# Kernel optimization log

Hardware: AMD Instinct MI355X
Metric: run time of the kernel (lower is better)

Reference implementation:

```python
import jax, jax.numpy as jnp
import numpy as np

D = 256; H = 8; DK = D // H
NT, NW, ND = 2000, 50000, 20000
E_TT, E_WT, E_TD, E_WD = 128000, 256000, 320000, 320000
SQRT_DK = float(np.sqrt(DK))


def setup_inputs() -> dict:
    key = jax.random.key(0)
    ks = jax.random.split(key, 32)
    def nrm(i, shape, s=0.05):
        return jax.random.normal(ks[i], shape, jnp.float32) * s
    inp = {
        "feat_topic": nrm(0, (NT, D), 1.0),
        "feat_word": nrm(1, (NW, D), 1.0),
        "feat_doc": nrm(2, (ND, D), 1.0),
        "ht_prev": nrm(3, (NT, D), 1.0),
        # stacked per-ntype linears, index: 0=topic, 1=word, 2=doc
        "Wk": nrm(4, (3, D, D)), "bk": nrm(5, (3, D)),
        "Wq": nrm(6, (3, D, D)), "bq": nrm(7, (3, D)),
        "Wv": nrm(8, (3, D, D)), "bv": nrm(9, (3, D)),
        # a_linears, index: 0=topic, 1=doc
        "Wa": nrm(10, (2, D, D)), "ba": nrm(11, (2, D)),
        "ln_g": jnp.ones((2, D), jnp.float32),
        "ln_b": jnp.zeros((2, D), jnp.float32),
        "skip": jnp.ones((2,), jnp.float32),
        # RNNCell for topic
        "Wih": nrm(12, (D, D)), "Whh": nrm(13, (D, D)),
        "bih": nrm(14, (D,)), "bhh": nrm(15, (D,)),
        # relation params, index: 0=tt, 1=wt, 2=td, 3=wd
        "rel_pri": jnp.ones((4, H), jnp.float32),
        "rel_att": nrm(16, (4, H, DK, DK), 0.1),
        "rel_msg": nrm(17, (4, H, DK, DK), 0.1),
        "src_tt": jax.random.randint(ks[18], (E_TT,), 0, NT),
        "dst_tt": jnp.arange(E_TT, dtype=jnp.int32) % NT,
        "src_wt": jax.random.randint(ks[19], (E_WT,), 0, NW),
        "dst_wt": jnp.arange(E_WT, dtype=jnp.int32) % NT,
        "src_td": jax.random.randint(ks[20], (E_TD,), 0, NT),
        "dst_td": jnp.arange(E_TD, dtype=jnp.int32) % ND,
        "src_wd": jax.random.randint(ks[21], (E_WD,), 0, NW),
        "dst_wd": jnp.arange(E_WD, dtype=jnp.int32) % ND,
    }
    return inp


def _proj(x, W, b):
    return (x @ W + b).reshape(-1, H, DK)


def _layernorm(x, g, b):
    mu = x.mean(-1, keepdims=True)
    var = ((x - mu) ** 2).mean(-1, keepdims=True)
    return (x - mu) * jax.lax.rsqrt(var + 1e-5) * g + b


def _rel_message(k, v, q, src, dst, pri, A_att, A_msg, n_dst):
    # k,v: [N_src,H,DK]; q: [N_dst,H,DK]; per-edge gather-compute-scatter
    key = jnp.einsum('ehd,hdo->eho', k[src], A_att)          # [E,H,DK]
    att = (q[dst] * key).sum(-1) * pri / SQRT_DK             # [E,H]
    val = jnp.einsum('ehd,hdo->eho', v[src], A_msg)          # [E,H,DK]
    m = jax.ops.segment_max(att, dst, num_segments=n_dst)
    e = jnp.exp(att - m[dst])
    s = jax.ops.segment_sum(e, dst, num_segments=n_dst)
    a = e / s[dst]                                           # edge softmax per dst
    t = jax.ops.segment_sum(a[..., None] * val, dst, num_segments=n_dst)
    return jax.nn.relu(t.reshape(n_dst, D))


def reference(feat_topic, feat_word, feat_doc, ht_prev, Wk, bk, Wq, bq, Wv, bv,
              Wa, ba, ln_g, ln_b, skip, Wih, Whh, bih, bhh,
              rel_pri, rel_att, rel_msg,
              src_tt, dst_tt, src_wt, dst_wt, src_td, dst_td, src_wd, dst_wd):
    # ---- phase 1: messages into topic nodes (etypes tt, wt) ----
    k_t = _proj(feat_topic, Wk[0], bk[0]); v_t = _proj(feat_topic, Wv[0], bv[0])
    k_w = _proj(feat_word,  Wk[1], bk[1]); v_w = _proj(feat_word,  Wv[1], bv[1])
    q_t = _proj(feat_topic, Wq[0], bq[0])
    t_tt = _rel_message(k_t, v_t, q_t, src_tt, dst_tt, rel_pri[0], rel_att[0], rel_msg[0], NT)
    t_wt = _rel_message(k_w, v_w, q_t, src_wt, dst_wt, rel_pri[1], rel_att[1], rel_msg[1], NT)
    t_topic = 0.5 * (t_tt + t_wt)                            # cross_reducer='mean'
    alpha = jax.nn.sigmoid(skip[0])
    trans = t_topic @ Wa[0] + ba[0]
    mix = trans * alpha + feat_topic * (1.0 - alpha)
    h = jnp.tanh(mix @ Wih + bih + ht_prev @ Whh + bhh)      # RNNCell
    topic_out = _layernorm(h, ln_g[0], ln_b[0])
    # ---- phase 2: messages into doc nodes (etypes td, wd), topic uses updated feats ----
    k_t2 = _proj(topic_out, Wk[0], bk[0]); v_t2 = _proj(topic_out, Wv[0], bv[0])
    q_d = _proj(feat_doc, Wq[2], bq[2])
    t_td = _rel_message(k_t2, v_t2, q_d, src_td, dst_td, rel_pri[2], rel_att[2], rel_msg[2], ND)
    t_wd = _rel_message(k_w, v_w, q_d, src_wd, dst_wd, rel_pri[3], rel_att[3], rel_msg[3], ND)
    t_doc = 0.5 * (t_td + t_wd)
    alpha2 = jax.nn.sigmoid(skip[1])
    trans2 = t_doc @ Wa[1] + ba[1]
    mix2 = trans2 * alpha2 + feat_doc * (1.0 - alpha2)
    doc_out = _layernorm(mix2, ln_g[1], ln_b[1])
    return topic_out, doc_out
```

## Files before the change

kernel.cpp:

```cpp
#include <hip/hip_runtime.h>
#include <hip/hip_bf16.h>
#include <hip/hip_fp8.h>

typedef __attribute__((ext_vector_type(8))) short bf16x8;
typedef __attribute__((ext_vector_type(4))) float f32x4;
typedef __attribute__((ext_vector_type(2))) float f32x2;

constexpr int NT = 2000, NW = 50000, ND = 20000;
constexpr float INV_SQRT_DK = 0.17677669529663687f;

__device__ inline float bfu(unsigned short u) {
    return __uint_as_float(((unsigned int)u) << 16);
}
__device__ inline float blo(unsigned int u) { return __uint_as_float(u << 16); }
__device__ inline float bhi(unsigned int u) { return __uint_as_float(u & 0xffff0000u); }
__device__ inline short f2bf(float x) {
    __hip_bfloat16 h = __float2bfloat16(x);
    short s; __builtin_memcpy(&s, &h, 2); return s;
}

__device__ inline void dec4(unsigned int w, float* o) {
#if __has_builtin(__builtin_amdgcn_cvt_pk_f32_fp8)
    f32x2 a = __builtin_amdgcn_cvt_pk_f32_fp8(w, false);
    f32x2 b = __builtin_amdgcn_cvt_pk_f32_fp8(w, true);
    o[0] = a[0]; o[1] = a[1]; o[2] = b[0]; o[3] = b[1];
#else
    __hip_fp8_e4m3 t0, t1, t2, t3;
    t0.__x = (__hip_fp8_storage_t)(w & 0xff);
    t1.__x = (__hip_fp8_storage_t)((w >> 8) & 0xff);
    t2.__x = (__hip_fp8_storage_t)((w >> 16) & 0xff);
    t3.__x = (__hip_fp8_storage_t)((w >> 24) & 0xff);
    o[0] = (float)t0; o[1] = (float)t1; o[2] = (float)t2; o[3] = (float)t3;
#endif
}
__device__ inline unsigned char f2fp8(float v) {
#if __has_builtin(__builtin_amdgcn_cvt_pk_fp8_f32)
    return (unsigned char)(__builtin_amdgcn_cvt_pk_fp8_f32(v, v, 0u, false) & 0xff);
#else
    __hip_fp8_e4m3 h(v); return (unsigned char)h.__x;
#endif
}

__device__ inline void cstore(float* p, float v) { *p = v; }
__device__ inline void cstore(short* p, float v) { *p = f2bf(v); }
__device__ inline void cstore(unsigned char* p, float v) { *p = f2fp8(v); }

__device__ inline void gload16(const short* g, short* l) {
    __builtin_amdgcn_global_load_lds(
        (const __attribute__((address_space(1))) void*)g,
        (__attribute__((address_space(3))) void*)l, 16, 0, 0);
}

__device__ inline float dot32f8(const unsigned char* __restrict__ kp, const float* __restrict__ qh) {
    const uint4 u = *reinterpret_cast<const uint4*>(kp);
    const uint4 v = *reinterpret_cast<const uint4*>(kp + 16);
    const unsigned int ws[8] = {u.x, u.y, u.z, u.w, v.x, v.y, v.z, v.w};
    float d = 0.f;
    #pragma unroll
    for (int c = 0; c < 8; ++c) {
        float f[4];
        dec4(ws[c], f);
        d += qh[c * 4 + 0] * f[0] + qh[c * 4 + 1] * f[1]
           + qh[c * 4 + 2] * f[2] + qh[c * 4 + 3] * f[3];
    }
    return d;
}

__global__ __launch_bounds__(256) void fold_kernel(
    const float* __restrict__ Wk, const float* __restrict__ bk,
    const float* __restrict__ Wv, const float* __restrict__ bv,
    const float* __restrict__ rel_att, const float* __restrict__ rel_msg,
    short* __restrict__ B_t1, short* __restrict__ B_w, short* __restrict__ B_t2,
    float* __restrict__ bias_t1, float* __restrict__ bias_w, float* __restrict__ bias_t2)
{
    const int f = blockIdx.x >> 3, chunk = blockIdx.x & 7;
    const int rel = f >> 1, isV = f & 1;
    const int ntype = (rel == 1 || rel == 3) ? 1 : 0;
    const float* Wsrc = (isV ? Wv : Wk) + ntype * 65536;
    const float* bsrc = (isV ? bv : bk) + ntype * 256;
    const float* A    = (isV ? rel_msg : rel_att) + rel * 8192;
    short* wdst; float* bdst;
    switch (f) {
        case 0: wdst = B_t1 + 65536;     bdst = bias_t1 + 256; break;
        case 1: wdst = B_t1 + 2 * 65536; bdst = bias_t1 + 512; break;
        case 2: wdst = B_w;              bdst = bias_w;        break;
        case 3: wdst = B_w + 65536;      bdst = bias_w + 256;  break;
        case 4: wdst = B_t2;             bdst = bias_t2;       break;
        case 5: wdst = B_t2 + 65536;     bdst = bias_t2 + 256; break;
        case 6: wdst = B_w + 2 * 65536;  bdst = bias_w + 512;  break;
        default: wdst = B_w + 3 * 65536; bdst = bias_w + 768;  break;
    }
    __shared__ float Wsh[32][256];
    const int tid = threadIdx.x;
    for (int i = 0; i < 32; ++i)
        Wsh[i][tid] = Wsrc[(chunk * 32 + i) * 256 + tid];
    __syncthreads();
    const int h = tid >> 5, o = tid & 31;
    float a[32];
    #pragma unroll
    for (int d = 0; d < 32; ++d) a[d] = A[h * 1024 + d * 32 + o];
    short tmp[32];
    #pragma unroll
    for (int r = 0; r < 32; ++r) {
        float s = 0.f;
        #pragma unroll
        for (int d = 0; d < 32; ++d) s = fmaf(Wsh[r][(h << 5) + d], a[d], s);
        tmp[r] = f2bf(s);
    }
    short* wp = wdst + tid * 256 + chunk * 32;
    #pragma unroll
    for (int r8 = 0; r8 < 4; ++r8) {
        bf16x8 v;
        #pragma unroll
        for (int t = 0; t < 8; ++t) v[t] = tmp[r8 * 8 + t];
        *reinterpret_cast<bf16x8*>(wp + r8 * 8) = v;
    }
    if (chunk == 0) {
        float s = 0.f;
        #pragma unroll
        for (int d = 0; d < 32; ++d) s = fmaf(bsrc[(h << 5) + d], a[d], s);
        bdst[tid] = s;
    }
}

struct TransP { const float* s[6]; short* d[6]; };
__global__ __launch_bounds__(256) void wtrans6(TransP p) {
    const int m = blockIdx.y, n = blockIdx.x, k = threadIdx.x;
    p.d[m][n * 256 + k] = f2bf(p.s[m][k * 256 + n]);
}

__global__ void copy_bias(const float* __restrict__ s, float* __restrict__ d) {
    d[threadIdx.x] = s[threadIdx.x];
}

template <bool XF32, typename OutT, int EPI, bool SWZ>
__global__ __launch_bounds__(256) void gemm_lds(
    const void* __restrict__ Xv, const short* __restrict__ Wt,
    const float* __restrict__ bias, OutT* __restrict__ C,
    int M, int ldc, const float* __restrict__ extra,
    const float* __restrict__ skipv, int skipIdx)
{
    __shared__ short As[128 * 64];
    __shared__ short Bs[128 * 64];
    int bxi = blockIdx.x, byi = blockIdx.y;
    if constexpr (SWZ) {
        const int h = bxi + (int)gridDim.x * byi;
        const int i = h >> 3;
        byi = (h & 7) + 8 * (i >> 3);
        bxi = i & 7;
        if (byi * 128 >= M) return;
    }
    const int tid = threadIdx.x;
    const int wave = tid >> 6, lane = tid & 63;
    const int wm = wave >> 1, wn = wave & 1;
    const int r = lane & 15, kb = lane >> 4;
    const int col0 = bxi * 128;
    const int row0 = byi * 128;

    const int l8 = lane >> 3;
    const int c8 = lane & 7;
    const int swz8 = c8 ^ l8;
    f32x4 acc[4][4] = {};

    for (int k0 = 0; k0 < 256; k0 += 64) {
        if (k0) __syncthreads();
        if constexpr (XF32) {
            #pragma unroll
            for (int q = 0; q < 4; ++q) {
                const int rl = wave * 32 + q * 8 + l8;
                const int grow = min(row0 + rl, M - 1);
                const float* xp = (const float*)Xv + grow * 256 + k0 + c8 * 8;
                const float4 x0 = *reinterpret_cast<const float4*>(xp);
                const float4 x1 = *reinterpret_cast<const float4*>(xp + 4);
                bf16x8 v;
                v[0] = f2bf(x0.x); v[1] = f2bf(x0.y); v[2] = f2bf(x0.z); v[3] = f2bf(x0.w);
                v[4] = f2bf(x1.x); v[5] = f2bf(x1.y); v[6] = f2bf(x1.z); v[7] = f2bf(x1.w);
                *reinterpret_cast<bf16x8*>(As + rl * 64 + swz8 * 8) = v;
            }
        } else {
            #pragma unroll
            for (int q = 0; q < 4; ++q) {
                const int rl = wave * 32 + q * 8 + l8;
                const int grow = min(row0 + rl, M - 1);
                gload16((const short*)Xv + grow * 256 + k0 + swz8 * 8,
                        As + (wave * 32 + q * 8) * 64);
            }
        }
        #pragma unroll
        for (int q = 0; q < 4; ++q) {
            const int cl = wave * 32 + q * 8 + l8;
            gload16(Wt + (col0 + cl) * 256 + k0 + swz8 * 8,
                    Bs + (wave * 32 + q * 8) * 64);
        }
        __syncthreads();
        #pragma unroll
        for (int s = 0; s < 2; ++s) {
            const int csw = ((kb + 4 * s) ^ (r & 7)) * 8;
            bf16x8 af[4], bw[4];
            #pragma unroll
            for (int i = 0; i < 4; ++i) {
                af[i] = *reinterpret_cast<const bf16x8*>(As + (wm * 64 + i * 16 + r) * 64 + csw);
                bw[i] = *reinterpret_cast<const bf16x8*>(Bs + (wn * 64 + i * 16 + r) * 64 + csw);
            }
            #pragma unroll
            for (int i = 0; i < 4; ++i)
                #pragma unroll
                for (int j = 0; j < 4; ++j)
                    acc[i][j] = __builtin_amdgcn_mfma_f32_16x16x32_bf16(af[i], bw[j], acc[i][j], 0, 0, 0);
        }
    }

    float alpha = 0.f;
    if (EPI == 1) alpha = 1.f / (1.f + __expf(-skipv[skipIdx]));
    #pragma unroll
    for (int i = 0; i < 4; ++i) {
        #pragma unroll
        for (int j = 0; j < 4; ++j) {
            const int col = col0 + wn * 64 + j * 16 + r;
            const float bc = bias[col];
            #pragma unroll
            for (int t = 0; t < 4; ++t) {
                const int rrow = row0 + wm * 64 + i * 16 + kb * 4 + t;
                if (rrow < M) {
                    float v = acc[i][j][t] + bc;
                    if (EPI == 1) v = alpha * v + (1.f - alpha) * extra[rrow * 256 + col];
                    if (EPI == 2) v = tanhf(v + extra[rrow * 256 + col]);
                    cstore(C + rrow * ldc + col, v);
                }
            }
        }
    }
}

template <int NE>
__device__ inline void rel_scores_f8(const unsigned char* __restrict__ kv, int ld, int koff,
                                     const int* __restrict__ sidx, int off, float scale,
                                     const float* __restrict__ qh, float* __restrict__ sc,
                                     int g, int l)
{
    constexpr int NL = NE / 32;
    float att[NL];
    #pragma unroll
    for (int t = 0; t < NL; ++t)
        att[t] = dot32f8(kv + (size_t)sidx[off + l + 32 * t] * ld + koff + g * 32, qh) * scale;
    float m = att[0];
    #pragma unroll
    for (int t = 1; t < NL; ++t) m = fmaxf(m, att[t]);
    #pragma unroll
    for (int o = 16; o > 0; o >>= 1) m = fmaxf(m, __shfl_xor(m, o));
    float ex[NL], s = 0.f;
    #pragma unroll
    for (int t = 0; t < NL; ++t) { ex[t] = __expf(att[t] - m); s += ex[t]; }
    #pragma unroll
    for (int o = 16; o > 0; o >>= 1) s += __shfl_xor(s, o);
    const float inv = 1.f / s;
    #pragma unroll
    for (int t = 0; t < NL; ++t) sc[(off + l + 32 * t) * 9 + g] = ex[t] * inv;
}

template <int NE>
__device__ inline void accum_f8(const unsigned char* __restrict__ kv, int ld, int voff,
                                const int* __restrict__ sidx, int off,
                                const float* __restrict__ sc,
                                int es, int ct, int h, float* __restrict__ acc)
{
    #pragma unroll
    for (int e = es; e < NE; e += 8) {
        const float w = sc[(off + e) * 9 + h];
        const uint2 u = *reinterpret_cast<const uint2*>(
            kv + (size_t)sidx[off + e] * ld + voff + ct * 8);
        float f[8];
        dec4(u.x, f); dec4(u.y, f + 4);
        #pragma unroll
        for (int k = 0; k < 8; ++k) acc[k] = fmaf(w, f[k], acc[k]);
    }
}

template <int NEA, int NEB>
__global__ __launch_bounds__(256) void msg_k(
    const short* __restrict__ q, int ldq,
    const unsigned char* __restrict__ kvA, int ldA, int koffA, int voffA,
    const int* __restrict__ srcA,
    const unsigned char* __restrict__ kvB, int ldB, int koffB, int voffB,
    const int* __restrict__ srcB,
    const float* __restrict__ relPri, int relA, int relB,
    short* __restrict__ out, int n_dst)
{
    constexpr int NET = NEA + NEB;
    const int j = blockIdx.x, tid = threadIdx.x;
    __shared__ float qsh[256];
    __shared__ int sidx[NET];
    __shared__ float sc[NET * 9];
    __shared__ float psA[8][256];
    __shared__ float psB[8][256];

    qsh[tid] = bfu((unsigned short)q[j * ldq + tid]);
    if (tid < NEA) sidx[tid] = srcA[j + tid * n_dst];
    else if (tid < NET) sidx[tid] = srcB[j + (tid - NEA) * n_dst];
    __syncthreads();

    const int g = tid >> 5, l = tid & 31;
    float qr[32];
    #pragma unroll
    for (int c = 0; c < 8; ++c) {
        const float4 v = *reinterpret_cast<const float4*>(qsh + g * 32 + c * 4);
        qr[c * 4] = v.x; qr[c * 4 + 1] = v.y; qr[c * 4 + 2] = v.z; qr[c * 4 + 3] = v.w;
    }

    if constexpr (NEA == 16 && NEB == 16) {
        const int isB = l >> 4;
        const unsigned char* base = isB ? kvB + koffB : kvA + koffA;
        const int ld = isB ? ldB : ldA;
        const float scale = relPri[(isB ? relB : relA) * 8 + g] * INV_SQRT_DK;
        const float att = dot32f8(base + (size_t)sidx[l] * ld + g * 32, qr) * scale;
        float m = att;
        #pragma unroll
        for (int o = 8; o > 0; o >>= 1) m = fmaxf(m, __shfl_xor(m, o));
        const float ex = __expf(att - m);
        float s = ex;
        #pragma unroll
        for (int o = 8; o > 0; o >>= 1) s += __shfl_xor(s, o);
        sc[l * 9 + g] = ex / s;
    } else {
        rel_scores_f8<NEA>(kvA, ldA, koffA, sidx, 0,
                           relPri[relA * 8 + g] * INV_SQRT_DK, qr, sc, g, l);
        rel_scores_f8<NEB>(kvB, ldB, koffB, sidx, NEA,
                           relPri[relB * 8 + g] * INV_SQRT_DK, qr, sc, g, l);
    }
    __syncthreads();

    const int es = tid >> 5, ct = tid & 31, hh = ct >> 2;
    float accA[8] = {}, accB[8] = {};
    accum_f8<NEA>(kvA, ldA, voffA, sidx, 0,   sc, es, ct, hh, accA);
    accum_f8<NEB>(kvB, ldB, voffB, sidx, NEA, sc, es, ct, hh, accB);
    const int sw = ct & 4;
    *reinterpret_cast<float4*>(&psA[es][(ct * 8) ^ sw])     = make_float4(accA[0], accA[1], accA[2], accA[3]);
    *reinterpret_cast<float4*>(&psA[es][(ct * 8 + 4) ^ sw]) = make_float4(accA[4], accA[5], accA[6], accA[7]);
    *reinterpret_cast<float4*>(&psB[es][(ct * 8) ^ sw])     = make_float4(accB[0], accB[1], accB[2], accB[3]);
    *reinterpret_cast<float4*>(&psB[es][(ct * 8 + 4) ^ sw]) = make_float4(accB[4], accB[5], accB[6], accB[7]);
    __syncthreads();

    float rA = 0.f, rB = 0.f;
    const int rp = tid ^ ((tid >> 3) & 4);
    #pragma unroll
    for (int e2 = 0; e2 < 8; ++e2) { rA += psA[e2][rp]; rB += psB[e2][rp]; }
    out[j * 256 + tid] = f2bf(0.5f * (fmaxf(rA, 0.f) + fmaxf(rB, 0.f)));
}

template <bool WB>
__global__ __launch_bounds__(256) void ln_k(
    float* __restrict__ data, const float* __restrict__ g,
    const float* __restrict__ b, int nrows, short* __restrict__ bfout)
{
    const int wid = threadIdx.x >> 6, lane = threadIdx.x & 63;
    const int row = blockIdx.x * 4 + wid;
    if (row >= nrows) return;
    float4 x = *reinterpret_cast<float4*>(data + row * 256 + lane * 4);
    float s  = x.x + x.y + x.z + x.w;
    float q2 = x.x * x.x + x.y * x.y + x.z * x.z + x.w * x.w;
    #pragma unroll
    for (int o = 32; o > 0; o >>= 1) { s += __shfl_xor(s, o); q2 += __shfl_xor(q2, o); }
    const float mu  = s * (1.f / 256.f);
    const float var = q2 * (1.f / 256.f) - mu * mu;
    const float rr = rsqrtf(var + 1e-5f);
    const float4 gg = *reinterpret_cast<const float4*>(g + lane * 4);
    const float4 bb = *reinterpret_cast<const float4*>(b + lane * 4);
    x.x = (x.x - mu) * rr * gg.x + bb.x;
    x.y = (x.y - mu) * rr * gg.y + bb.y;
    x.z = (x.z - mu) * rr * gg.z + bb.z;
    x.w = (x.w - mu) * rr * gg.w + bb.w;
    *reinterpret_cast<float4*>(data + row * 256 + lane * 4) = x;
    if (WB) {
        ushort4 u;
        u.x = (unsigned short)f2bf(x.x); u.y = (unsigned short)f2bf(x.y);
        u.z = (unsigned short)f2bf(x.z); u.w = (unsigned short)f2bf(x.w);
        *reinterpret_cast<ushort4*>((unsigned short*)bfout + row * 256 + lane * 4) = u;
    }
}

extern "C" void kernel_launch(void* const* d_in, const int* in_sizes, int n_in,
                              void* d_out, int out_size, void* d_ws, size_t ws_size,
                              hipStream_t stream)
{
    const float* feat_topic = (const float*)d_in[0];
    const float* feat_word  = (const float*)d_in[1];
    const float* feat_doc   = (const float*)d_in[2];
    const float* ht_prev    = (const float*)d_in[3];
    const float* Wk  = (const float*)d_in[4];
    const float* bk  = (const float*)d_in[5];
    const float* Wq  = (const float*)d_in[6];
    const float* bq  = (const float*)d_in[7];
    const float* Wv  = (const float*)d_in[8];
    const float* bv  = (const float*)d_in[9];
    const float* Wa  = (const float*)d_in[10];
    const float* ba  = (const float*)d_in[11];
    const float* ln_g = (const float*)d_in[12];
    const float* ln_b = (const float*)d_in[13];
    const float* skip = (const float*)d_in[14];
    const float* Wih  = (const float*)d_in[15];
    const float* Whh  = (const float*)d_in[16];
    const float* bih  = (const float*)d_in[17];
    const float* bhh  = (const float*)d_in[18];
    const float* rel_pri = (const float*)d_in[19];
    const float* rel_att = (const float*)d_in[20];
    const float* rel_msg = (const float*)d_in[21];
    const int* src_tt = (const int*)d_in[22];
    const int* src_wt = (const int*)d_in[24];
    const int* src_td = (const int*)d_in[26];
    const int* src_wd = (const int*)d_in[28];

    short* B_t1 = (short*)d_ws;
    short* B_w  = B_t1 + 196608;
    short* B_t2 = B_w + 262144;
    short* Wq2t = B_t2 + 131072;
    short* Whht = Wq2t + 65536;
    short* Wa0t = Whht + 65536;
    short* Wiht = Wa0t + 65536;
    short* Wa1t = Wiht + 65536;
    short* q_t  = Wa1t + 65536;
    unsigned char* kv1 = (unsigned char*)(q_t + 512000);
    unsigned char* w8  = kv1 + 1024000;
    unsigned char* kv2 = w8 + 51200000;
    short* qd   = (short*)(kv2 + 1024000);
    short* ttop = qd + 5120000;
    short* mixb = ttop + 512000;
    short* tdoc = mixb + 512000;
    short* xt2  = tdoc + 5120000;
    float* bias_t1 = (float*)(xt2 + 512000);
    float* bias_w  = bias_t1 + 768;
    float* bias_t2 = bias_w + 1024;
    float* r2      = bias_t2 + 512;

    float* out_topic = (float*)d_out;
    float* out_doc   = out_topic + NT * 256;

    fold_kernel<<<dim3(64), 256, 0, stream>>>(Wk, bk, Wv, bv, rel_att, rel_msg,
                                              B_t1, B_w, B_t2, bias_t1, bias_w, bias_t2);
    TransP tp;
    tp.s[0] = Wq;            tp.d[0] = B_t1;
    tp.s[1] = Wq + 131072;   tp.d[1] = Wq2t;
    tp.s[2] = Whh;           tp.d[2] = Whht;
    tp.s[3] = Wih;           tp.d[3] = Wiht;
    tp.s[4] = Wa;            tp.d[4] = Wa0t;
    tp.s[5] = Wa + 65536;    tp.d[5] = Wa1t;
    wtrans6<<<dim3(256, 6), 256, 0, stream>>>(tp);
    copy_bias<<<dim3(1), 256, 0, stream>>>(bq, bias_t1);

    gemm_lds<true, unsigned char, 0, true><<<dim3(8, 392), 256, 0, stream>>>(
        feat_word, B_w, bias_w, w8, NW, 1024, nullptr, nullptr, 0);

    gemm_lds<true, short, 0, false><<<dim3(2, 16), 256, 0, stream>>>(
        feat_topic, B_t1, bias_t1, q_t, NT, 256, nullptr, nullptr, 0);
    gemm_lds<true, unsigned char, 0, false><<<dim3(4, 16), 256, 0, stream>>>(
        feat_topic, B_t1 + 65536, bias_t1 + 256, kv1, NT, 512, nullptr, nullptr, 0);
    gemm_lds<true, short, 0, false><<<dim3(2, 157), 256, 0, stream>>>(
        feat_doc, Wq2t, bq + 512, qd, ND, 256, nullptr, nullptr, 0);
    gemm_lds<true, float, 0, false><<<dim3(2, 16), 256, 0, stream>>>(
        ht_prev, Whht, bhh, r2, NT, 256, nullptr, nullptr, 0);

    msg_k<64, 128><<<dim3(NT), 256, 0, stream>>>(
        q_t, 256,
        kv1, 512, 0, 256, src_tt,
        w8, 1024, 0, 256, src_wt,
        rel_pri, 0, 1, ttop, NT);

    gemm_lds<false, short, 1, false><<<dim3(2, 16), 256, 0, stream>>>(
        ttop, Wa0t, ba, mixb, NT, 256, feat_topic, skip, 0);
    gemm_lds<false, float, 2, false><<<dim3(2, 16), 256, 0, stream>>>(
        mixb, Wiht, bih, out_topic, NT, 256, r2, nullptr, 0);
    ln_k<true><<<dim3(500), 256, 0, stream>>>(out_topic, ln_g, ln_b, NT, xt2);

    gemm_lds<false, unsigned char, 0, false><<<dim3(4, 16), 256, 0, stream>>>(
        xt2, B_t2, bias_t2, kv2, NT, 512, nullptr, nullptr, 0);

    msg_k<16, 16><<<dim3(ND), 256, 0, stream>>>(
        qd, 256,
        kv2, 512, 0, 256, src_td,
        w8, 1024, 512, 768, src_wd,
        rel_pri, 2, 3, tdoc, ND);

    gemm_lds<false, float, 1, false><<<dim3(2, 157), 256, 0, stream>>>(
        tdoc, Wa1t, ba + 256, out_doc, ND, 256, feat_doc, skip, 1);
    ln_k<false><<<dim3(5000), 256, 0, stream>>>(out_doc, ln_g + 256, ln_b + 256, ND, nullptr);
}
```

Measured before the change: 311.6 us.

## Double-buffer LDS tiles in GEMM with register prefetch of next K-slice

Replaces the single-buffered 64-wide K-step GEMM with a double-buffered pipeline over 32-wide K-slices. Global loads for the next slice (async LDS loads for bf16, register prefetch for fp32 inputs) are issued before the MFMA work on the current buffer, with one barrier per step. The LDS layout changes to a smaller swizzle, and fp32 A tiles use padded rows. This aims to hide global memory latency behind compute, at the cost of more barriers per tile and more registers for the prefetch.

```diff
diff --git a/kernel.cpp b/kernel.cpp
--- a/kernel.cpp
+++ b/kernel.cpp
@@ -134,14 +134,15 @@
 }
 
 template <bool XF32, typename OutT, int EPI, bool SWZ>
-__global__ __launch_bounds__(256) void gemm_lds(
+__global__ __launch_bounds__(256) void gemm_db(
     const void* __restrict__ Xv, const short* __restrict__ Wt,
     const float* __restrict__ bias, OutT* __restrict__ C,
     int M, int ldc, const float* __restrict__ extra,
     const float* __restrict__ skipv, int skipIdx)
 {
-    __shared__ short As[128 * 64];
-    __shared__ short Bs[128 * 64];
+    constexpr int LDA = XF32 ? 36 : 32;
+    __shared__ short As[2][128 * LDA];
+    __shared__ short Bs[2][128 * 32];
     int bxi = blockIdx.x, byi = blockIdx.y;
     if constexpr (SWZ) {
         const int h = bxi + (int)gridDim.x * byi;
@@ -154,61 +155,91 @@
     const int wave = tid >> 6, lane = tid & 63;
     const int wm = wave >> 1, wn = wave & 1;
     const int r = lane & 15, kb = lane >> 4;
-    const int col0 = bxi * 128;
-    const int row0 = byi * 128;
-
-    const int l8 = lane >> 3;
-    const int c8 = lane & 7;
-    const int swz8 = c8 ^ l8;
+    const int col0 = bxi * 128, row0 = byi * 128;
+
+    const int srow = lane >> 2;
+    const int sc8  = lane & 3;
+    const int swz  = (lane >> 3) & 3;
+    const int gc8  = sc8 ^ swz;
+    const int rsw  = (r >> 1) & 3;
+    const int aslot = XF32 ? kb : (kb ^ rsw);
+    const int bslot = kb ^ rsw;
+
     f32x4 acc[4][4] = {};
-
-    for (int k0 = 0; k0 < 256; k0 += 64) {
-        if (k0) __syncthreads();
-        if constexpr (XF32) {
+    float4 pf[4];
+
+    auto stageB = [&](int t, int b) {
+        const int k0 = t * 32;
+        #pragma unroll
+        for (int q2 = 0; q2 < 2; ++q2) {
+            const int cl = wave * 32 + q2 * 16;
+            gload16(Wt + (col0 + cl + srow) * 256 + k0 + gc8 * 8,
+                    &Bs[b][cl * 32]);
+        }
+    };
+    auto stageA16 = [&](int t, int b) {
+        const int k0 = t * 32;
+        #pragma unroll
+        for (int q2 = 0; q2 < 2; ++q2) {
+            const int rl = wave * 32 + q2 * 16;
+            const int grow = min(row0 + rl + srow, M - 1);
+            gload16((const short*)Xv + grow * 256 + k0 + gc8 * 8,
+                    &As[b][rl * 32]);
+        }
+    };
+    auto stageAf_load = [&](int t) {
+        const int k0 = t * 32;
+        #pragma unroll
+        for (int q2 = 0; q2 < 2; ++q2) {
+            const int grow = min(row0 + wave * 32 + q2 * 16 + srow, M - 1);
+            const float* xp = (const float*)Xv + grow * 256 + k0 + sc8 * 8;
+            pf[q2 * 2]     = *reinterpret_cast<const float4*>(xp);
+            pf[q2 * 2 + 1] = *reinterpret_cast<const float4*>(xp + 4);
+        }
+    };
+    auto stageAf_write = [&](int b) {
+        #pragma unroll
+        for (int q2 = 0; q2 < 2; ++q2) {
+            const float4 x0 = pf[q2 * 2], x1 = pf[q2 * 2 + 1];
+            bf16x8 v;
+            v[0] = f2bf(x0.x); v[1] = f2bf(x0.y); v[2] = f2bf(x0.z); v[3] = f2bf(x0.w);
+            v[4] = f2bf(x1.x); v[5] = f2bf(x1.y); v[6] = f2bf(x1.z); v[7] = f2bf(x1.w);
+            *reinterpret_cast<bf16x8*>(
+                &As[b][(wave * 32 + q2 * 16 + srow) * 36 + sc8 * 8]) = v;
+        }
+    };
+    auto compute = [&](int b) {
+        bf16x8 af[4], bw[4];
+        #pragma unroll
+        for (int i = 0; i < 4; ++i) {
+            af[i] = *reinterpret_cast<const bf16x8*>(
+                &As[b][(wm * 64 + i * 16 + r) * LDA + aslot * 8]);
+            bw[i] = *reinterpret_cast<const bf16x8*>(
+                &Bs[b][(wn * 64 + i * 16 + r) * 32 + bslot * 8]);
+        }
+        #pragma unroll
+        for (int i = 0; i < 4; ++i)
             #pragma unroll
-            for (int q = 0; q < 4; ++q) {
-                const int rl = wave * 32 + q * 8 + l8;
-                const int grow = min(row0 + rl, M - 1);
-                const float* xp = (const float*)Xv + grow * 256 + k0 + c8 * 8;
-                const float4 x0 = *reinterpret_cast<const float4*>(xp);
-                const float4 x1 = *reinterpret_cast<const float4*>(xp + 4);
-                bf16x8 v;
-                v[0] = f2bf(x0.x); v[1] = f2bf(x0.y); v[2] = f2bf(x0.z); v[3] = f2bf(x0.w);
-                v[4] = f2bf(x1.x); v[5] = f2bf(x1.y); v[6] = f2bf(x1.z); v[7] = f2bf(x1.w);
-                *reinterpret_cast<bf16x8*>(As + rl * 64 + swz8 * 8) = v;
-            }
-        } else {
-            #pragma unroll
-            for (int q = 0; q < 4; ++q) {
-                const int rl = wave * 32 + q * 8 + l8;
-                const int grow = min(row0 + rl, M - 1);
-                gload16((const short*)Xv + grow * 256 + k0 + swz8 * 8,
-                        As + (wave * 32 + q * 8) * 64);
-            }
-        }
-        #pragma unroll
-        for (int q = 0; q < 4; ++q) {
-            const int cl = wave * 32 + q * 8 + l8;
-            gload16(Wt + (col0 + cl) * 256 + k0 + swz8 * 8,
-                    Bs + (wave * 32 + q * 8) * 64);
-        }
+            for (int j = 0; j < 4; ++j)
+                acc[i][j] = __builtin_amdgcn_mfma_f32_16x16x32_bf16(af[i], bw[j], acc[i][j], 0, 0, 0);
+    };
+
+    if constexpr (XF32) { stageAf_load(0); stageAf_write(0); }
+    else stageA16(0, 0);
+    stageB(0, 0);
+    __syncthreads();
+    int cur = 0;
+    #pragma unroll
+    for (int t = 0; t < 7; ++t) {
+        if constexpr (XF32) stageAf_load(t + 1);
+        stageB(t + 1, cur ^ 1);
+        if constexpr (!XF32) stageA16(t + 1, cur ^ 1);
+        compute(cur);
+        if constexpr (XF32) stageAf_write(cur ^ 1);
         __syncthreads();
-        #pragma unroll
-        for (int s = 0; s < 2; ++s) {
-            const int csw = ((kb + 4 * s) ^ (r & 7)) * 8;
-            bf16x8 af[4], bw[4];
-            #pragma unroll
-            for (int i = 0; i < 4; ++i) {
-                af[i] = *reinterpret_cast<const bf16x8*>(As + (wm * 64 + i * 16 + r) * 64 + csw);
-                bw[i] = *reinterpret_cast<const bf16x8*>(Bs + (wn * 64 + i * 16 + r) * 64 + csw);
-            }
-            #pragma unroll
-            for (int i = 0; i < 4; ++i)
-                #pragma unroll
-                for (int j = 0; j < 4; ++j)
-                    acc[i][j] = __builtin_amdgcn_mfma_f32_16x16x32_bf16(af[i], bw[j], acc[i][j], 0, 0, 0);
-        }
-    }
+        cur ^= 1;
+    }
+    compute(cur);
 
     float alpha = 0.f;
     if (EPI == 1) alpha = 1.f / (1.f + __expf(-skipv[skipIdx]));
@@ -446,16 +477,16 @@
     wtrans6<<<dim3(256, 6), 256, 0, stream>>>(tp);
     copy_bias<<<dim3(1), 256, 0, stream>>>(bq, bias_t1);
 
-    gemm_lds<true, unsigned char, 0, true><<<dim3(8, 392), 256, 0, stream>>>(
+    gemm_db<true, unsigned char, 0, true><<<dim3(8, 392), 256, 0, stream>>>(
         feat_word, B_w, bias_w, w8, NW, 1024, nullptr, nullptr, 0);
 
-    gemm_lds<true, short, 0, false><<<dim3(2, 16), 256, 0, stream>>>(
+    gemm_db<true, short, 0, false><<<dim3(2, 16), 256, 0, stream>>>(
         feat_topic, B_t1, bias_t1, q_t, NT, 256, nullptr, nullptr, 0);
-    gemm_lds<true, unsigned char, 0, false><<<dim3(4, 16), 256, 0, stream>>>(
+    gemm_db<true, unsigned char, 0, false><<<dim3(4, 16), 256, 0, stream>>>(
         feat_topic, B_t1 + 65536, bias_t1 + 256, kv1, NT, 512, nullptr, nullptr, 0);
-    gemm_lds<true, short, 0, false><<<dim3(2, 157), 256, 0, stream>>>(
+    gemm_db<true, short, 0, false><<<dim3(2, 157), 256, 0, stream>>>(
         feat_doc, Wq2t, bq + 512, qd, ND, 256, nullptr, nullptr, 0);
-    gemm_lds<true, float, 0, false><<<dim3(2, 16), 256, 0, stream>>>(
+    gemm_db<true, float, 0, false><<<dim3(2, 16), 256, 0, stream>>>(
         ht_prev, Whht, bhh, r2, NT, 256, nullptr, nullptr, 0);
 
     msg_k<64, 128><<<dim3(NT), 256, 0, stream>>>(
@@ -464,13 +495,13 @@
         w8, 1024, 0, 256, src_wt,
         rel_pri, 0, 1, ttop, NT);
 
-    gemm_lds<false, short, 1, false><<<dim3(2, 16), 256, 0, stream>>>(
+    gemm_db<false, short, 1, false><<<dim3(2, 16), 256, 0, stream>>>(
         ttop, Wa0t, ba, mixb, NT, 256, feat_topic, skip, 0);
-    gemm_lds<false, float, 2, false><<<dim3(2, 16), 256, 0, stream>>>(
+    gemm_db<false, float, 2, false><<<dim3(2, 16), 256, 0, stream>>>(
         mixb, Wiht, bih, out_topic, NT, 256, r2, nullptr, 0);
     ln_k<true><<<dim3(500), 256, 0, stream>>>(out_topic, ln_g, ln_b, NT, xt2);
 
-    gemm_lds<false, unsigned char, 0, false><<<dim3(4, 16), 256, 0, stream>>>(
+    gemm_db<false, unsigned char, 0, false><<<dim3(4, 16), 256, 0, stream>>>(
         xt2, B_t2, bias_t2, kv2, NT, 512, nullptr, nullptr, 0);
 
     msg_k<16, 16><<<dim3(ND), 256, 0, stream>>>(
@@ -479,7 +510,7 @@
         w8, 1024, 512, 768, src_wd,
         rel_pri, 2, 3, tdoc, ND);
 
-    gemm_lds<false, float, 1, false><<<dim3(2, 157), 256, 0, stream>>>(
+    gemm_db<false, float, 1, false><<<dim3(2, 157), 256, 0, stream>>>(
         tdoc, Wa1t, ba + 256, out_doc, ND, 256, feat_doc, skip, 1);
     ln_k<false><<<dim3(5000), 256, 0, stream>>>(out_doc, ln_g + 256, ln_b + 256, ND, nullptr);
 }
```

After: 327.5 us. 1.05x slower.

## Double-buffer LDS tiles in GEMM kernel to overlap loads with MFMA

Applied to the files above, without the earlier changes.

Converts the LDS-tiled bf16 GEMM into a double-buffered pipeline: the next K-tile's A and B loads are issued into a second shared buffer (fp32 inputs are prefetched into registers and converted after compute) while MFMAs run on the current buffer. This removes one barrier per K step and hides global-load latency behind compute. It doubles LDS use to 64 KB per block and adds prefetch registers, which may reduce occupancy. With only 4 K-steps, little latency is left to hide.

```diff
diff --git a/kernel.cpp b/kernel.cpp
--- a/kernel.cpp
+++ b/kernel.cpp
@@ -134,14 +134,14 @@
 }
 
 template <bool XF32, typename OutT, int EPI, bool SWZ>
-__global__ __launch_bounds__(256) void gemm_lds(
+__global__ __launch_bounds__(256) void gemm_db(
     const void* __restrict__ Xv, const short* __restrict__ Wt,
     const float* __restrict__ bias, OutT* __restrict__ C,
     int M, int ldc, const float* __restrict__ extra,
     const float* __restrict__ skipv, int skipIdx)
 {
-    __shared__ short As[128 * 64];
-    __shared__ short Bs[128 * 64];
+    __shared__ short As[2][128 * 64];
+    __shared__ short Bs[2][128 * 64];
     int bxi = blockIdx.x, byi = blockIdx.y;
     if constexpr (SWZ) {
         const int h = bxi + (int)gridDim.x * byi;
@@ -161,46 +161,58 @@
     const int c8 = lane & 7;
     const int swz8 = c8 ^ l8;
     f32x4 acc[4][4] = {};
-
-    for (int k0 = 0; k0 < 256; k0 += 64) {
-        if (k0) __syncthreads();
-        if constexpr (XF32) {
-            #pragma unroll
-            for (int q = 0; q < 4; ++q) {
-                const int rl = wave * 32 + q * 8 + l8;
-                const int grow = min(row0 + rl, M - 1);
-                const float* xp = (const float*)Xv + grow * 256 + k0 + c8 * 8;
-                const float4 x0 = *reinterpret_cast<const float4*>(xp);
-                const float4 x1 = *reinterpret_cast<const float4*>(xp + 4);
-                bf16x8 v;
-                v[0] = f2bf(x0.x); v[1] = f2bf(x0.y); v[2] = f2bf(x0.z); v[3] = f2bf(x0.w);
-                v[4] = f2bf(x1.x); v[5] = f2bf(x1.y); v[6] = f2bf(x1.z); v[7] = f2bf(x1.w);
-                *reinterpret_cast<bf16x8*>(As + rl * 64 + swz8 * 8) = v;
-            }
-        } else {
-            #pragma unroll
-            for (int q = 0; q < 4; ++q) {
-                const int rl = wave * 32 + q * 8 + l8;
-                const int grow = min(row0 + rl, M - 1);
-                gload16((const short*)Xv + grow * 256 + k0 + swz8 * 8,
-                        As + (wave * 32 + q * 8) * 64);
-            }
-        }
+    float4 pf[8];
+
+    auto stageB = [&](int t, int b) {
+        const int k0 = t * 64;
         #pragma unroll
         for (int q = 0; q < 4; ++q) {
             const int cl = wave * 32 + q * 8 + l8;
             gload16(Wt + (col0 + cl) * 256 + k0 + swz8 * 8,
-                    Bs + (wave * 32 + q * 8) * 64);
+                    &Bs[b][(wave * 32 + q * 8) * 64]);
         }
-        __syncthreads();
+    };
+    auto stageA16 = [&](int t, int b) {
+        const int k0 = t * 64;
+        #pragma unroll
+        for (int q = 0; q < 4; ++q) {
+            const int rl = wave * 32 + q * 8 + l8;
+            const int grow = min(row0 + rl, M - 1);
+            gload16((const short*)Xv + grow * 256 + k0 + swz8 * 8,
+                    &As[b][(wave * 32 + q * 8) * 64]);
+        }
+    };
+    auto stageAf_load = [&](int t) {
+        const int k0 = t * 64;
+        #pragma unroll
+        for (int q = 0; q < 4; ++q) {
+            const int rl = wave * 32 + q * 8 + l8;
+            const int grow = min(row0 + rl, M - 1);
+            const float* xp = (const float*)Xv + grow * 256 + k0 + c8 * 8;
+            pf[q * 2]     = *reinterpret_cast<const float4*>(xp);
+            pf[q * 2 + 1] = *reinterpret_cast<const float4*>(xp + 4);
+        }
+    };
+    auto stageAf_write = [&](int b) {
+        #pragma unroll
+        for (int q = 0; q < 4; ++q) {
+            const int rl = wave * 32 + q * 8 + l8;
+            const float4 x0 = pf[q * 2], x1 = pf[q * 2 + 1];
+            bf16x8 v;
+            v[0] = f2bf(x0.x); v[1] = f2bf(x0.y); v[2] = f2bf(x0.z); v[3] = f2bf(x0.w);
+            v[4] = f2bf(x1.x); v[5] = f2bf(x1.y); v[6] = f2bf(x1.z); v[7] = f2bf(x1.w);
+            *reinterpret_cast<bf16x8*>(&As[b][rl * 64 + swz8 * 8]) = v;
+        }
+    };
+    auto compute = [&](int b) {
         #pragma unroll
         for (int s = 0; s < 2; ++s) {
             const int csw = ((kb + 4 * s) ^ (r & 7)) * 8;
             bf16x8 af[4], bw[4];
             #pragma unroll
             for (int i = 0; i < 4; ++i) {
-                af[i] = *reinterpret_cast<const bf16x8*>(As + (wm * 64 + i * 16 + r) * 64 + csw);
-                bw[i] = *reinterpret_cast<const bf16x8*>(Bs + (wn * 64 + i * 16 + r) * 64 + csw);
+                af[i] = *reinterpret_cast<const bf16x8*>(&As[b][(wm * 64 + i * 16 + r) * 64 + csw]);
+                bw[i] = *reinterpret_cast<const bf16x8*>(&Bs[b][(wn * 64 + i * 16 + r) * 64 + csw]);
             }
             #pragma unroll
             for (int i = 0; i < 4; ++i)
@@ -208,7 +220,24 @@
                 for (int j = 0; j < 4; ++j)
                     acc[i][j] = __builtin_amdgcn_mfma_f32_16x16x32_bf16(af[i], bw[j], acc[i][j], 0, 0, 0);
         }
-    }
+    };
+
+    if constexpr (XF32) { stageAf_load(0); stageAf_write(0); }
+    else stageA16(0, 0);
+    stageB(0, 0);
+    __syncthreads();
+    int cur = 0;
+    #pragma unroll
+    for (int t = 0; t < 3; ++t) {
+        if constexpr (XF32) stageAf_load(t + 1);
+        else stageA16(t + 1, cur ^ 1);
+        stageB(t + 1, cur ^ 1);
+        compute(cur);
+        if constexpr (XF32) stageAf_write(cur ^ 1);
+        __syncthreads();
+        cur ^= 1;
+    }
+    compute(cur);
 
     float alpha = 0.f;
     if (EPI == 1) alpha = 1.f / (1.f + __expf(-skipv[skipIdx]));
@@ -446,16 +475,16 @@
     wtrans6<<<dim3(256, 6), 256, 0, stream>>>(tp);
     copy_bias<<<dim3(1), 256, 0, stream>>>(bq, bias_t1);
 
-    gemm_lds<true, unsigned char, 0, true><<<dim3(8, 392), 256, 0, stream>>>(
+    gemm_db<true, unsigned char, 0, true><<<dim3(8, 392), 256, 0, stream>>>(
         feat_word, B_w, bias_w, w8, NW, 1024, nullptr, nullptr, 0);
 
-    gemm_lds<true, short, 0, false><<<dim3(2, 16), 256, 0, stream>>>(
+    gemm_db<true, short, 0, false><<<dim3(2, 16), 256, 0, stream>>>(
         feat_topic, B_t1, bias_t1, q_t, NT, 256, nullptr, nullptr, 0);
-    gemm_lds<true, unsigned char, 0, false><<<dim3(4, 16), 256, 0, stream>>>(
+    gemm_db<true, unsigned char, 0, false><<<dim3(4, 16), 256, 0, stream>>>(
         feat_topic, B_t1 + 65536, bias_t1 + 256, kv1, NT, 512, nullptr, nullptr, 0);
-    gemm_lds<true, short, 0, false><<<dim3(2, 157), 256, 0, stream>>>(
+    gemm_db<true, short, 0, false><<<dim3(2, 157), 256, 0, stream>>>(
         feat_doc, Wq2t, bq + 512, qd, ND, 256, nullptr, nullptr, 0);
-    gemm_lds<true, float, 0, false><<<dim3(2, 16), 256, 0, stream>>>(
+    gemm_db<true, float, 0, false><<<dim3(2, 16), 256, 0, stream>>>(
         ht_prev, Whht, bhh, r2, NT, 256, nullptr, nullptr, 0);
 
     msg_k<64, 128><<<dim3(NT), 256, 0, stream>>>(
@@ -464,13 +493,13 @@
         w8, 1024, 0, 256, src_wt,
         rel_pri, 0, 1, ttop, NT);
 
-    gemm_lds<false, short, 1, false><<<dim3(2, 16), 256, 0, stream>>>(
+    gemm_db<false, short, 1, false><<<dim3(2, 16), 256, 0, stream>>>(
         ttop, Wa0t, ba, mixb, NT, 256, feat_topic, skip, 0);
-    gemm_lds<false, float, 2, false><<<dim3(2, 16), 256, 0, stream>>>(
+    gemm_db<false, float, 2, false><<<dim3(2, 16), 256, 0, stream>>>(
         mixb, Wiht, bih, out_topic, NT, 256, r2, nullptr, 0);
     ln_k<true><<<dim3(500), 256, 0, stream>>>(out_topic, ln_g, ln_b, NT, xt2);
 
-    gemm_lds<false, unsigned char, 0, false><<<dim3(4, 16), 256, 0, stream>>>(
+    gemm_db<false, unsigned char, 0, false><<<dim3(4, 16), 256, 0, stream>>>(
         xt2, B_t2, bias_t2, kv2, NT, 512, nullptr, nullptr, 0);
 
     msg_k<16, 16><<<dim3(ND), 256, 0, stream>>>(
@@ -479,7 +508,7 @@
         w8, 1024, 512, 768, src_wd,
         rel_pri, 2, 3, tdoc, ND);
 
-    gemm_lds<false, float, 1, false><<<dim3(2, 157), 256, 0, stream>>>(
+    gemm_db<false, float, 1, false><<<dim3(2, 157), 256, 0, stream>>>(
         tdoc, Wa1t, ba + 256, out_doc, ND, 256, feat_doc, skip, 1);
     ln_k<false><<<dim3(5000), 256, 0, stream>>>(out_doc, ln_g + 256, ln_b + 256, ND, nullptr);
 }
```

After: 327.5 us. 5.1% more time.
